# Kernel optimization log

Measured on AMD Instinct MI355X. Metric: run time of the kernel, lower is better.

## Reference

```python
import jax, jax.numpy as jnp
import numpy as np

N = 50000
E = 800000
D = 128
L = 2


def setup_inputs() -> dict:
    key = jax.random.key(0)
    k0, k1, k2 = jax.random.split(key, 3)
    x = jax.random.normal(k0, (N, D), dtype=jnp.float32)
    edge_index = jax.random.randint(k1, (2, E), 0, N, dtype=jnp.int64)
    # GCNConv weights: one [D, D] matrix + bias per layer (dim_in -> dim_in)
    W = jax.random.normal(k2, (L, D, D), dtype=jnp.float32) * (1.0 / np.sqrt(D))
    b = jnp.zeros((L, D), dtype=jnp.float32)
    return {"x": x, "edge_index": edge_index, "W": W, "b": b}


def reference(x, edge_index, W, b):
    """Stacked GCNConv + relu (dropout is identity in eval mode).

    GCNConv: out = D^{-1/2} (A + I) D^{-1/2} (X W) + b, with self-loops added.
    """
    n = x.shape[0]
    loops = jnp.arange(n, dtype=edge_index.dtype)
    src = jnp.concatenate([edge_index[0], loops])  # [E + N]
    dst = jnp.concatenate([edge_index[1], loops])  # [E + N]
    # Degree (with self-loops) based symmetric normalization
    deg = jax.ops.segment_sum(jnp.ones_like(dst, dtype=x.dtype), dst, num_segments=n)
    dinv = jax.lax.rsqrt(deg)  # deg >= 1 thanks to self-loops
    coef = (dinv[src] * dinv[dst])[:, None]  # [E + N, 1]

    num_layers = W.shape[0]
    for i in range(num_layers):
        h = x @ W[i]  # transform first, as PyG GCNConv does
        x = jax.ops.segment_sum(h[src] * coef, dst, num_segments=n) + b[i]
        x = jax.nn.relu(x)
        # F.dropout with training=False is identity
    return x
```

## Files before the change

### kernel.cpp

```cpp
#include <hip/hip_runtime.h>
#include <hip/hip_fp16.h>


#define D 128
#define WP 136
#define YP 136
#define ABI 6
#define AGT 32
#define NB_SCAN 196

typedef _Float16 half8 __attribute__((ext_vector_type(8)));
typedef float floatx4 __attribute__((ext_vector_type(4)));


__global__ void count_kernel(const int* __restrict__ dst, int* deg8,
                             int* __restrict__ rank, int e, int n) {
    int i = blockIdx.x * blockDim.x + threadIdx.x;
    int c = (blockIdx.x & 7) * n;
    if (i < e) rank[i] = atomicAdd(&deg8[c + dst[i]], 1);
}

__global__ __launch_bounds__(256) void scanA_cvtw_kernel(const int* __restrict__ deg8,
                                                         int* __restrict__ degT,
                                                         int* __restrict__ base8,
                                                         int* __restrict__ partial,
                                                         int n, int nbs,
                                                         const float* __restrict__ W,
                                                         __half* __restrict__ WhT) {
    __shared__ int red[4];
    int tid = threadIdx.x;
    int bid = blockIdx.x;
    if (bid < nbs) {
        int i = bid * 256 + tid;
        int tot = 0;
        if (i < n) {
            int run = 0;
#pragma unroll
            for (int c = 0; c < 8; ++c) {
                base8[c * n + i] = run;
                run += deg8[c * n + i];
            }
            degT[i] = run;
            tot = run;
        }
        for (int off = 32; off > 0; off >>= 1) tot += __shfl_down(tot, off, 64);
        if ((tid & 63) == 0) red[tid >> 6] = tot;
        __syncthreads();
        if (tid == 0) partial[bid] = red[0] + red[1] + red[2] + red[3];
    } else {
        int id = (bid - nbs) * 256 + tid;
        int l = id >> 14;
        int rem = id & 16383;
        int f = rem >> 7;
        int k = rem & 127;
        WhT[id] = __float2half(W[l * 16384 + k * 128 + f]);
    }
}

__global__ __launch_bounds__(256) void scanC2_kernel(const int* __restrict__ degT,
                                                     const int* __restrict__ partial,
                                                     int* __restrict__ row_ptr,
                                                     float* __restrict__ dinv, int n) {
    __shared__ int sc[256];
    __shared__ int scb[256];
    int tid = threadIdx.x;
    int bid = blockIdx.x;
    int p = (tid < NB_SCAN) ? partial[tid] : 0;
    scb[tid] = p;
    __syncthreads();
    for (int off = 1; off < 256; off <<= 1) {
        int v = (tid >= off) ? scb[tid - off] : 0;
        __syncthreads();
        scb[tid] += v;
        __syncthreads();
    }
    int i = bid * 256 + tid;
    int c = (i < n) ? degT[i] : 0;
    sc[tid] = c;
    __syncthreads();
    for (int off = 1; off < 256; off <<= 1) {
        int v = (tid >= off) ? sc[tid - off] : 0;
        __syncthreads();
        sc[tid] += v;
        __syncthreads();
    }
    if (i < n) {
        int base = ((bid == 0) ? 0 : scb[bid - 1]) + sc[tid] - c;
        row_ptr[i] = base;
        dinv[i] = rsqrtf((float)(c + 1));
    }
    if (bid == 0 && tid == 0) row_ptr[n] = scb[NB_SCAN - 1];
}


__device__ inline void gemm_body(int bid, int tid,
                                 const float* __restrict__ Xf,
                                 const __half* __restrict__ WhT,
                                 __half* __restrict__ Hh, int n,
                                 _Float16* wlds) {
#pragma unroll
    for (int q = 0; q < 8; ++q) {
        int idx = tid + q * 256;
        int row = idx >> 4;
        int col8 = (idx & 15) * 8;
        const uint2* gsrc = (const uint2*)(WhT + row * 128 + col8);
        uint2 a = gsrc[0];
        uint2 b = gsrc[1];
        uint2* ldst = (uint2*)(wlds + row * WP + col8);
        ldst[0] = a;
        ldst[1] = b;
    }
    __syncthreads();

    const int wave = tid >> 6;
    const int lane = tid & 63;
    const int m = lane & 15;
    const int quad = lane >> 4;

    const int node = bid * 64 + wave * 16 + m;
    const int node_ld = node < n ? node : (n - 1);

    half8 bfr[4];
#pragma unroll
    for (int k = 0; k < 4; ++k) {
        const float4* p = (const float4*)(Xf + (size_t)node_ld * 128 + k * 32 + quad * 8);
        float4 lo = p[0];
        float4 hi = p[1];
        half8 h;
        h[0] = (_Float16)lo.x; h[1] = (_Float16)lo.y;
        h[2] = (_Float16)lo.z; h[3] = (_Float16)lo.w;
        h[4] = (_Float16)hi.x; h[5] = (_Float16)hi.y;
        h[6] = (_Float16)hi.z; h[7] = (_Float16)hi.w;
        bfr[k] = h;
    }

    floatx4 acc[8];
#pragma unroll
    for (int f = 0; f < 8; ++f) acc[f] = (floatx4){0.f, 0.f, 0.f, 0.f};

#pragma unroll
    for (int f = 0; f < 8; ++f) {
#pragma unroll
        for (int k = 0; k < 4; ++k) {
            half8 a = *(const half8*)(wlds + (f * 16 + m) * WP + k * 32 + quad * 8);
            acc[f] = __builtin_amdgcn_mfma_f32_16x16x32_f16(a, bfr[k], acc[f], 0, 0, 0);
        }
    }

    if (node < n) {
#pragma unroll
        for (int f = 0; f < 8; ++f) {
            __half2 p0 = __floats2half2_rn(acc[f][0], acc[f][1]);
            __half2 p1 = __floats2half2_rn(acc[f][2], acc[f][3]);
            uint2 pk;
            pk.x = *(unsigned int*)&p0;
            pk.y = *(unsigned int*)&p1;
            *(uint2*)(Hh + (size_t)node * 128 + f * 16 + quad * 4) = pk;
        }
    }
}

__device__ inline void fill_body(int i,
                                 const int* __restrict__ src,
                                 const int* __restrict__ dst,
                                 const int* __restrict__ rank,
                                 const int* __restrict__ row_ptr,
                                 const int* __restrict__ base8,
                                 const float* __restrict__ dinv,
                                 int2* __restrict__ recs, int e, int n) {
    if (i < e) {
        int d = dst[i];
        int s = src[i];
        int c = (i >> 8) & 7;
        int pos = row_ptr[d] + base8[c * n + d] + rank[i];
        int2 rec;
        rec.x = s;
        rec.y = __float_as_int(dinv[s] * dinv[d]);
        recs[pos] = rec;
    }
}


__global__ __launch_bounds__(256) void gemmfill_kernel(const float* __restrict__ Xf,
                                                       const __half* __restrict__ WhT,
                                                       __half* __restrict__ Hh, int n, int nbg,
                                                       const int* __restrict__ src,
                                                       const int* __restrict__ dst,
                                                       const int* __restrict__ rank,
                                                       const int* __restrict__ row_ptr,
                                                       const int* __restrict__ base8,
                                                       const float* __restrict__ dinv,
                                                       int2* __restrict__ recs, int e) {
    __shared__ _Float16 wlds[128 * WP];
    int bid = blockIdx.x;
    int tid = threadIdx.x;
    if (bid < nbg) {
        gemm_body(bid, tid, Xf, WhT, Hh, n, wlds);
    } else {
        fill_body((bid - nbg) * 256 + tid, src, dst, rank, row_ptr, base8, dinv, recs, e, n);
    }
}


__device__ inline void unpack8(uint4 u, float* f) {
    union { unsigned int x; __half2 h; } a, b, c, d;
    a.x = u.x; b.x = u.y; c.x = u.z; d.x = u.w;
    float2 f0 = __half22float2(a.h);
    float2 f1 = __half22float2(b.h);
    float2 f2 = __half22float2(c.h);
    float2 f3 = __half22float2(d.h);
    f[0] = f0.x; f[1] = f0.y; f[2] = f1.x; f[3] = f1.y;
    f[4] = f2.x; f[5] = f2.y; f[6] = f3.x; f[7] = f3.y;
}

__device__ inline void agg_row(int v, int qw, int fl,
                               const uint4* __restrict__ H16,
                               const int2* __restrict__ recs,
                               const int* __restrict__ row_ptr,
                               const float* __restrict__ dinv,
                               float* acc) {
    {
        float di = dinv[v];
        float selfc = (qw == 0) ? di * di : 0.f;
        uint4 hv = H16[(size_t)v * 16 + fl];
        float f[8]; unpack8(hv, f);
#pragma unroll
        for (int t = 0; t < 8; ++t) acc[t] = f[t] * selfc;
    }

    int e0 = row_ptr[v];
    int e1 = row_ptr[v + 1];
    int e = e0;
    for (; e + 4 * ABI <= e1; e += 4 * ABI) {
        int2 r[ABI]; uint4 hu[ABI];
#pragma unroll
        for (int j = 0; j < ABI; ++j) r[j] = recs[e + 4 * j + qw];
#pragma unroll
        for (int j = 0; j < ABI; ++j) hu[j] = H16[(size_t)r[j].x * 16 + fl];
#pragma unroll
        for (int j = 0; j < ABI; ++j) {
            float c = __int_as_float(r[j].y);
            float f[8]; unpack8(hu[j], f);
#pragma unroll
            for (int t = 0; t < 8; ++t) acc[t] = fmaf(f[t], c, acc[t]);
        }
    }
    if (e < e1) {
        int2 r[ABI]; uint4 hu[ABI]; bool act[ABI];
#pragma unroll
        for (int j = 0; j < ABI; ++j) {
            int idx = e + 4 * j + qw;
            act[j] = idx < e1;
            if (act[j]) r[j] = recs[idx];
        }
#pragma unroll
        for (int j = 0; j < ABI; ++j) {
            if (act[j]) hu[j] = H16[(size_t)r[j].x * 16 + fl];
        }
#pragma unroll
        for (int j = 0; j < ABI; ++j) {
            if (act[j]) {
                float c = __int_as_float(r[j].y);
                float f[8]; unpack8(hu[j], f);
#pragma unroll
                for (int t = 0; t < 8; ++t) acc[t] = fmaf(f[t], c, acc[t]);
            }
        }
    }
}

__global__ __launch_bounds__(256) void agg_kernel(const __half* __restrict__ H,
                                                  const int2* __restrict__ recs,
                                                  const int* __restrict__ row_ptr,
                                                  const float* __restrict__ dinv,
                                                  const float* __restrict__ bias,
                                                  float* __restrict__ YF, int n) {
    int wave = threadIdx.x >> 6;
    int lane = threadIdx.x & 63;
    int v = blockIdx.x * 4 + wave;
    if (v >= n) return;

    const int qw = lane >> 4;
    const int fl = lane & 15;
    const uint4* H16 = (const uint4*)H;

    float acc[8];
    agg_row(v, qw, fl, H16, recs, row_ptr, dinv, acc);

#pragma unroll
    for (int t = 0; t < 8; ++t) {
        acc[t] += __shfl_xor(acc[t], 16);
        acc[t] += __shfl_xor(acc[t], 32);
    }

    if (qw == 0) {
        const float4* B4 = (const float4*)bias;
        float4 b0 = B4[fl * 2];
        float4 b1 = B4[fl * 2 + 1];
        float4* Y4 = (float4*)YF;
        Y4[(size_t)v * 32 + fl * 2] = make_float4(
            fmaxf(acc[0] + b0.x, 0.f), fmaxf(acc[1] + b0.y, 0.f),
            fmaxf(acc[2] + b0.z, 0.f), fmaxf(acc[3] + b0.w, 0.f));
        Y4[(size_t)v * 32 + fl * 2 + 1] = make_float4(
            fmaxf(acc[4] + b1.x, 0.f), fmaxf(acc[5] + b1.y, 0.f),
            fmaxf(acc[6] + b1.z, 0.f), fmaxf(acc[7] + b1.w, 0.f));
    }
}

__global__ __launch_bounds__(512, 8) void aggemm_kernel(
    const __half* __restrict__ H,
    const int2* __restrict__ recs,
    const int* __restrict__ row_ptr,
    const float* __restrict__ dinv,
    const float* __restrict__ bias,
    const __half* __restrict__ WhT2,
    __half* __restrict__ H2, int n) {
    __shared__ _Float16 yt[AGT * YP];
    const int tid = threadIdx.x;
    const int wave = tid >> 6;
    const int lane = tid & 63;
    const int qw = lane >> 4;
    const int fl = lane & 15;
    const int g = blockIdx.x;
    const uint4* H16 = (const uint4*)H;

    const float4* B4 = (const float4*)bias;
    float4 b0 = B4[fl * 2];
    float4 b1 = B4[fl * 2 + 1];
#pragma unroll 1
    for (int it = 0; it < 4; ++it) {
        int r = wave * 4 + it;
        int v = g * AGT + r;
        if (v < n) {
            float acc[8];
            agg_row(v, qw, fl, H16, recs, row_ptr, dinv, acc);
#pragma unroll
            for (int t = 0; t < 8; ++t) {
                acc[t] += __shfl_xor(acc[t], 16);
                acc[t] += __shfl_xor(acc[t], 32);
            }
            if (qw == 0) {
                __half2 p0 = __floats2half2_rn(fmaxf(acc[0] + b0.x, 0.f), fmaxf(acc[1] + b0.y, 0.f));
                __half2 p1 = __floats2half2_rn(fmaxf(acc[2] + b0.z, 0.f), fmaxf(acc[3] + b0.w, 0.f));
                __half2 p2 = __floats2half2_rn(fmaxf(acc[4] + b1.x, 0.f), fmaxf(acc[5] + b1.y, 0.f));
                __half2 p3 = __floats2half2_rn(fmaxf(acc[6] + b1.z, 0.f), fmaxf(acc[7] + b1.w, 0.f));
                uint4 pk;
                pk.x = *(unsigned int*)&p0;
                pk.y = *(unsigned int*)&p1;
                pk.z = *(unsigned int*)&p2;
                pk.w = *(unsigned int*)&p3;
                *(uint4*)&yt[r * YP + fl * 8] = pk;
            }
        } else if (qw == 0) {
            uint4 z = make_uint4(0, 0, 0, 0);
            *(uint4*)&yt[r * YP + fl * 8] = z;
        }
    }
    __syncthreads();

    const int mg = wave & 1;
    const int fh = wave >> 1;
    const int node = g * AGT + mg * 16 + fl;

    half8 bfr[4];
#pragma unroll
    for (int k = 0; k < 4; ++k)
        bfr[k] = *(const half8*)&yt[(mg * 16 + fl) * YP + k * 32 + qw * 8];

#pragma unroll
    for (int fb = 0; fb < 2; ++fb) {
        int f = fh * 2 + fb;
        floatx4 a4 = (floatx4){0.f, 0.f, 0.f, 0.f};
#pragma unroll
        for (int k = 0; k < 4; ++k) {
            half8 a = *(const half8*)(WhT2 + ((f * 16 + fl) * 128 + k * 32 + qw * 8));
            a4 = __builtin_amdgcn_mfma_f32_16x16x32_f16(a, bfr[k], a4, 0, 0, 0);
        }
        if (node < n) {
            __half2 p0 = __floats2half2_rn(a4[0], a4[1]);
            __half2 p1 = __floats2half2_rn(a4[2], a4[3]);
            uint2 pk;
            pk.x = *(unsigned int*)&p0;
            pk.y = *(unsigned int*)&p1;
            *(uint2*)(H2 + (size_t)node * 128 + f * 16 + qw * 4) = pk;
        }
    }
}


extern "C" void kernel_launch(void* const* d_in, const int* in_sizes, int n_in,
                              void* d_out, int out_size, void* d_ws, size_t ws_size,
                              hipStream_t stream) {
    const float* x = (const float*)d_in[0];
    const int* ei = (const int*)d_in[1];
    const float* W = (const float*)d_in[2];
    const float* b = (const float*)d_in[3];
    float* out = (float*)d_out;

    const int N = in_sizes[0] / D;
    const int E = in_sizes[1] / 2;

    const int* src = ei;
    const int* dst = ei + E;

    int* wsi = (int*)d_ws;
    float* wsf = (float*)d_ws;
    const size_t o_deg8 = 0;
    const size_t o_degT = o_deg8 + 400000;
    const size_t o_dinv = o_degT + 50000;
    const size_t o_rp   = o_dinv + 50000;
    const size_t o_part = o_rp + 50016;
    const size_t o_boff = o_part + 256;
    const size_t o_b8   = o_boff + 256;
    const size_t o_rank = o_b8 + 400000;
    const size_t o_rec  = o_rank + 800000;
    const size_t o_h    = o_rec + 1600000;
    const size_t o_wht  = o_h + 3200000;
    const size_t o_h2   = o_wht + 16384;

    int* deg8    = wsi + o_deg8;
    int* degT    = wsi + o_degT;
    float* dinv  = wsf + o_dinv;
    int* row_ptr = wsi + o_rp;
    int* partial = wsi + o_part;
    int* base8   = wsi + o_b8;
    int* rank    = wsi + o_rank;
    int2* recs   = (int2*)(wsi + o_rec);
    __half* h    = (__half*)(wsi + o_h);
    __half* wht  = (__half*)(wsi + o_wht);
    __half* h2   = (__half*)(wsi + o_h2);

    const int nb_e = (E + 255) / 256;
    const int nb_s = (N + 255) / 256;
    const int nb_g = (N + 63) / 64;
    const int nb_ag = (N + AGT - 1) / AGT;
    const int nb_a = (N + 3) / 4;

    hipMemsetAsync(deg8, 0, (size_t)8 * 50000 * sizeof(int), stream);
    count_kernel<<<nb_e, 256, 0, stream>>>(dst, deg8, rank, E, N);
    scanA_cvtw_kernel<<<nb_s + 128, 256, 0, stream>>>(deg8, degT, base8, partial,
                                                      N, nb_s, W, wht);
    scanC2_kernel<<<nb_s, 256, 0, stream>>>(degT, partial, row_ptr, dinv, N);
    gemmfill_kernel<<<nb_g + nb_e, 256, 0, stream>>>(x, wht, h, N, nb_g,
                                                     src, dst, rank, row_ptr, base8,
                                                     dinv, recs, E);
    aggemm_kernel<<<nb_ag, 512, 0, stream>>>(h, recs, row_ptr, dinv, b,
                                             wht + 16384, h2, N);
    agg_kernel<<<nb_a, 256, 0, stream>>>(h2, recs, row_ptr, dinv, b + D, out, N);
}
```

Baseline: 232.8 us.

## Assign one node per 16-lane quarter-wave in aggregation instead of per wave

The aggregation kernels now map each 16-lane quarter of a wavefront to its own destination node, which walks its edge list sequentially, instead of splitting one node's edges across four quarters and reducing with cross-lane shuffles. This removes the shuffle reduction and the idle lanes on low-degree nodes (average degree is about 16). The unroll depth per quarter rises from 6 to 8 to keep enough gathers in flight, and launch bounds and grid sizes are adjusted. The risk is load imbalance between quarters that get nodes of different degree, plus longer serial chains per node.

```diff
diff --git a/kernel.cpp b/kernel.cpp
--- a/kernel.cpp
+++ b/kernel.cpp
@@ -5,7 +5,7 @@
 #define D 128
 #define WP 136
 #define YP 136
-#define ABI 6
+#define ABI 8
 #define AGT 32
 #define NB_SCAN 196
 
@@ -213,15 +213,15 @@
     f[4] = f2.x; f[5] = f2.y; f[6] = f3.x; f[7] = f3.y;
 }
 
-__device__ inline void agg_row(int v, int qw, int fl,
-                               const uint4* __restrict__ H16,
-                               const int2* __restrict__ recs,
-                               const int* __restrict__ row_ptr,
-                               const float* __restrict__ dinv,
-                               float* acc) {
+__device__ inline void agg_row_q(int v, int fl,
+                                 const uint4* __restrict__ H16,
+                                 const int2* __restrict__ recs,
+                                 const int* __restrict__ row_ptr,
+                                 const float* __restrict__ dinv,
+                                 float* acc) {
     {
         float di = dinv[v];
-        float selfc = (qw == 0) ? di * di : 0.f;
+        float selfc = di * di;
         uint4 hv = H16[(size_t)v * 16 + fl];
         float f[8]; unpack8(hv, f);
 #pragma unroll
@@ -231,10 +231,10 @@
     int e0 = row_ptr[v];
     int e1 = row_ptr[v + 1];
     int e = e0;
-    for (; e + 4 * ABI <= e1; e += 4 * ABI) {
+    for (; e + ABI <= e1; e += ABI) {
         int2 r[ABI]; uint4 hu[ABI];
 #pragma unroll
-        for (int j = 0; j < ABI; ++j) r[j] = recs[e + 4 * j + qw];
+        for (int j = 0; j < ABI; ++j) r[j] = recs[e + j];
 #pragma unroll
         for (int j = 0; j < ABI; ++j) hu[j] = H16[(size_t)r[j].x * 16 + fl];
 #pragma unroll
@@ -249,9 +249,8 @@
         int2 r[ABI]; uint4 hu[ABI]; bool act[ABI];
 #pragma unroll
         for (int j = 0; j < ABI; ++j) {
-            int idx = e + 4 * j + qw;
-            act[j] = idx < e1;
-            if (act[j]) r[j] = recs[idx];
+            act[j] = (e + j) < e1;
+            if (act[j]) r[j] = recs[e + j];
         }
 #pragma unroll
         for (int j = 0; j < ABI; ++j) {
@@ -269,45 +268,36 @@
     }
 }
 
-__global__ __launch_bounds__(256) void agg_kernel(const __half* __restrict__ H,
-                                                  const int2* __restrict__ recs,
-                                                  const int* __restrict__ row_ptr,
-                                                  const float* __restrict__ dinv,
-                                                  const float* __restrict__ bias,
-                                                  float* __restrict__ YF, int n) {
+__global__ __launch_bounds__(256, 4) void agg_kernel(const __half* __restrict__ H,
+                                                     const int2* __restrict__ recs,
+                                                     const int* __restrict__ row_ptr,
+                                                     const float* __restrict__ dinv,
+                                                     const float* __restrict__ bias,
+                                                     float* __restrict__ YF, int n) {
     int wave = threadIdx.x >> 6;
     int lane = threadIdx.x & 63;
-    int v = blockIdx.x * 4 + wave;
+    int qw = lane >> 4;
+    int fl = lane & 15;
+    int v = blockIdx.x * 16 + wave * 4 + qw;
     if (v >= n) return;
 
-    const int qw = lane >> 4;
-    const int fl = lane & 15;
     const uint4* H16 = (const uint4*)H;
-
     float acc[8];
-    agg_row(v, qw, fl, H16, recs, row_ptr, dinv, acc);
-
-#pragma unroll
-    for (int t = 0; t < 8; ++t) {
-        acc[t] += __shfl_xor(acc[t], 16);
-        acc[t] += __shfl_xor(acc[t], 32);
-    }
-
-    if (qw == 0) {
-        const float4* B4 = (const float4*)bias;
-        float4 b0 = B4[fl * 2];
-        float4 b1 = B4[fl * 2 + 1];
-        float4* Y4 = (float4*)YF;
-        Y4[(size_t)v * 32 + fl * 2] = make_float4(
-            fmaxf(acc[0] + b0.x, 0.f), fmaxf(acc[1] + b0.y, 0.f),
-            fmaxf(acc[2] + b0.z, 0.f), fmaxf(acc[3] + b0.w, 0.f));
-        Y4[(size_t)v * 32 + fl * 2 + 1] = make_float4(
-            fmaxf(acc[4] + b1.x, 0.f), fmaxf(acc[5] + b1.y, 0.f),
-            fmaxf(acc[6] + b1.z, 0.f), fmaxf(acc[7] + b1.w, 0.f));
-    }
-}
-
-__global__ __launch_bounds__(512, 8) void aggemm_kernel(
+    agg_row_q(v, fl, H16, recs, row_ptr, dinv, acc);
+
+    const float4* B4 = (const float4*)bias;
+    float4 b0 = B4[fl * 2];
+    float4 b1 = B4[fl * 2 + 1];
+    float4* Y4 = (float4*)YF;
+    Y4[(size_t)v * 32 + fl * 2] = make_float4(
+        fmaxf(acc[0] + b0.x, 0.f), fmaxf(acc[1] + b0.y, 0.f),
+        fmaxf(acc[2] + b0.z, 0.f), fmaxf(acc[3] + b0.w, 0.f));
+    Y4[(size_t)v * 32 + fl * 2 + 1] = make_float4(
+        fmaxf(acc[4] + b1.x, 0.f), fmaxf(acc[5] + b1.y, 0.f),
+        fmaxf(acc[6] + b1.z, 0.f), fmaxf(acc[7] + b1.w, 0.f));
+}
+
+__global__ __launch_bounds__(512, 4) void aggemm_kernel(
     const __half* __restrict__ H,
     const int2* __restrict__ recs,
     const int* __restrict__ row_ptr,
@@ -324,34 +314,26 @@
     const int g = blockIdx.x;
     const uint4* H16 = (const uint4*)H;
 
-    const float4* B4 = (const float4*)bias;
-    float4 b0 = B4[fl * 2];
-    float4 b1 = B4[fl * 2 + 1];
-#pragma unroll 1
-    for (int it = 0; it < 4; ++it) {
-        int r = wave * 4 + it;
+    {
+        const float4* B4 = (const float4*)bias;
+        float4 b0 = B4[fl * 2];
+        float4 b1 = B4[fl * 2 + 1];
+        int r = wave * 4 + qw;
         int v = g * AGT + r;
         if (v < n) {
             float acc[8];
-            agg_row(v, qw, fl, H16, recs, row_ptr, dinv, acc);
-#pragma unroll
-            for (int t = 0; t < 8; ++t) {
-                acc[t] += __shfl_xor(acc[t], 16);
-                acc[t] += __shfl_xor(acc[t], 32);
-            }
-            if (qw == 0) {
-                __half2 p0 = __floats2half2_rn(fmaxf(acc[0] + b0.x, 0.f), fmaxf(acc[1] + b0.y, 0.f));
-                __half2 p1 = __floats2half2_rn(fmaxf(acc[2] + b0.z, 0.f), fmaxf(acc[3] + b0.w, 0.f));
-                __half2 p2 = __floats2half2_rn(fmaxf(acc[4] + b1.x, 0.f), fmaxf(acc[5] + b1.y, 0.f));
-                __half2 p3 = __floats2half2_rn(fmaxf(acc[6] + b1.z, 0.f), fmaxf(acc[7] + b1.w, 0.f));
-                uint4 pk;
-                pk.x = *(unsigned int*)&p0;
-                pk.y = *(unsigned int*)&p1;
-                pk.z = *(unsigned int*)&p2;
-                pk.w = *(unsigned int*)&p3;
-                *(uint4*)&yt[r * YP + fl * 8] = pk;
-            }
-        } else if (qw == 0) {
+            agg_row_q(v, fl, H16, recs, row_ptr, dinv, acc);
+            __half2 p0 = __floats2half2_rn(fmaxf(acc[0] + b0.x, 0.f), fmaxf(acc[1] + b0.y, 0.f));
+            __half2 p1 = __floats2half2_rn(fmaxf(acc[2] + b0.z, 0.f), fmaxf(acc[3] + b0.w, 0.f));
+            __half2 p2 = __floats2half2_rn(fmaxf(acc[4] + b1.x, 0.f), fmaxf(acc[5] + b1.y, 0.f));
+            __half2 p3 = __floats2half2_rn(fmaxf(acc[6] + b1.z, 0.f), fmaxf(acc[7] + b1.w, 0.f));
+            uint4 pk;
+            pk.x = *(unsigned int*)&p0;
+            pk.y = *(unsigned int*)&p1;
+            pk.z = *(unsigned int*)&p2;
+            pk.w = *(unsigned int*)&p3;
+            *(uint4*)&yt[r * YP + fl * 8] = pk;
+        } else {
             uint4 z = make_uint4(0, 0, 0, 0);
             *(uint4*)&yt[r * YP + fl * 8] = z;
         }
@@ -434,7 +416,7 @@
     const int nb_s = (N + 255) / 256;
     const int nb_g = (N + 63) / 64;
     const int nb_ag = (N + AGT - 1) / AGT;
-    const int nb_a = (N + 3) / 4;
+    const int nb_a = (N + 15) / 16;
 
     hipMemsetAsync(deg8, 0, (size_t)8 * 50000 * sizeof(int), stream);
     count_kernel<<<nb_e, 256, 0, stream>>>(dst, deg8, rank, E, N);
```

Result: faster. 218.1 us, median of 2 (-6.3%).
